# Kernel optimization log

Hardware: AMD Instinct MI355X
Metric: run time of the kernel (lower is better)

The kernel has to match this reference:

```python
import jax, jax.numpy as jnp
import numpy as np

M_MAX = 8
GN_GROUPS = 8  # _pick_gn_groups(64)
HEADS = 4
G_C = 19
PER_C = 16


def silu(x):
    return x * jax.nn.sigmoid(x)


def layer_norm(x, g, b, eps=1e-5):
    mu = x.mean(-1, keepdims=True)
    var = ((x - mu) ** 2).mean(-1, keepdims=True)
    return (x - mu) * jax.lax.rsqrt(var + eps) * g + b


def group_norm(x, g, b, eps=1e-5):
    N, C, H, W = x.shape
    xr = x.reshape(N, GN_GROUPS, C // GN_GROUPS, H, W)
    mu = xr.mean((2, 3, 4), keepdims=True)
    var = ((xr - mu) ** 2).mean((2, 3, 4), keepdims=True)
    xn = ((xr - mu) * jax.lax.rsqrt(var + eps)).reshape(N, C, H, W)
    return xn * g[:, None, None] + b[:, None, None]


def conv1x1(x, w):  # x [N,C,H,W], w [O,C]
    return jnp.einsum('nchw,oc->nohw', x, w)


def dw3x3(x, w):  # depthwise 3x3, w [C,1,3,3]
    return jax.lax.conv_general_dilated(x, w, (1, 1), 'SAME', feature_group_count=x.shape[1], dimension_numbers=('NCHW', 'OIHW', 'NCHW'))


def forward(board, stem_w, stem_g, stem_b, qw, qb, kw, kb, vw, vb, ow, ob, ln_g, ln_b, dw_w, gn1_g, gn1_b, pw_w, gn2_g, gn2_b, pol_w, pol_b, vh_w1, vh_b1, vh_w2, vh_b2, om_w, om_b, op_w1, op_b1, op_w2, op_b2):
    B, Cin, H, W = board.shape
    hid = stem_w.shape[0]
    hd = hid // HEADS
    g = board[:, :G_C]
    p = board[:, G_C:G_C + M_MAX * PER_C].reshape(B, M_MAX, PER_C, H, W)
    player_in = jnp.concatenate([jnp.broadcast_to(g[:, None], (B, M_MAX, G_C, H, W)), p], axis=2)
    x = conv1x1(player_in.reshape(B * M_MAX, G_C + PER_C, H, W), stem_w)
    x = silu(group_norm(x, stem_g, stem_b)).reshape(B, M_MAX, hid, H, W)
    m_each = jnp.argmax(board[:, 7:14, 0, 0], axis=1) + 2  # number of players in [2,8]
    present = jnp.arange(M_MAX) < m_each[:, None]  # [B, M_MAX] bool
    neg = jnp.finfo(board.dtype).min
    L = qw.shape[0]
    for i in range(L):
        tokens = x.transpose(0, 3, 4, 1, 2).reshape(B, H * W, M_MAX, hid)
        q = (tokens @ qw[i].T + qb[i]).reshape(B, H * W, M_MAX, HEADS, hd)
        k = (tokens @ kw[i].T + kb[i]).reshape(B, H * W, M_MAX, HEADS, hd)
        v = (tokens @ vw[i].T + vb[i]).reshape(B, H * W, M_MAX, HEADS, hd)
        logits = jnp.einsum('bnqhd,bnkhd->bnhqk', q, k) * (hd ** -0.5)
        logits = jnp.where(present[:, None, None, None, :], logits, neg)
        attn = jax.nn.softmax(logits, axis=-1)
        ao = jnp.einsum('bnhqk,bnkhd->bnqhd', attn, v).reshape(B, H * W, M_MAX, hid)
        tokens = layer_norm(tokens + ao @ ow[i].T + ob[i], ln_g[i], ln_b[i])
        xc = tokens.reshape(B, H, W, M_MAX, hid).transpose(0, 3, 4, 1, 2).reshape(B * M_MAX, hid, H, W)
        y = silu(group_norm(dw3x3(xc, dw_w[i]), gn1_g[i], gn1_b[i]))
        y = group_norm(conv1x1(y, pw_w[i]), gn2_g[i], gn2_b[i])
        xc = silu(xc + y)
        x = xc.reshape(B, M_MAX, hid, H, W) * present[:, :, None, None, None].astype(xc.dtype)
    x0 = x[:, 0]
    logits_p = (conv1x1(x0, pol_w) + pol_b[:, None, None]).reshape(B, H * W)
    pooled0 = x0.mean((2, 3))
    value = (silu(pooled0 @ vh_w1.T + vh_b1) @ vh_w2.T + vh_b2)[:, 0]
    move_all = (conv1x1(x.reshape(B * M_MAX, hid, H, W), om_w) + om_b[:, None, None]).reshape(B, M_MAX, M_MAX, H * W)
    pooled_all = x.mean((3, 4))
    param_all = (silu(pooled_all @ op_w1.T + op_b1) @ op_w2.T + op_b2).reshape(B, M_MAX, M_MAX, 5)
    idx = jnp.arange(M_MAX)
    pf = present[..., None]
    opp_move = move_all[:, idx, idx, :] * pf.astype(move_all.dtype)
    opp_param = param_all[:, idx, idx, :] * pf.astype(param_all.dtype)
    return (logits_p, value, opp_move, opp_param)


def setup_inputs() -> dict:
    key = jax.random.key(0)
    ks = iter(jax.random.split(key, 48))
    def rn(shape, s=0.1):
        return jax.random.normal(next(ks), shape, jnp.float32) * s
    B, H, W, C, L = 16, 32, 32, 64, 6
    inp = {
        'board': jax.random.normal(next(ks), (B, 149, H, W), jnp.float32),
        'stem_w': rn((C, 35)), 'stem_g': jnp.ones((C,)), 'stem_b': jnp.zeros((C,)),
        'qw': rn((L, C, C)), 'qb': rn((L, C), 0.01),
        'kw': rn((L, C, C)), 'kb': rn((L, C), 0.01),
        'vw': rn((L, C, C)), 'vb': rn((L, C), 0.01),
        'ow': rn((L, C, C)), 'ob': rn((L, C), 0.01),
        'ln_g': jnp.ones((L, C)), 'ln_b': jnp.zeros((L, C)),
        'dw_w': rn((L, C, 1, 3, 3)),
        'gn1_g': jnp.ones((L, C)), 'gn1_b': jnp.zeros((L, C)),
        'pw_w': rn((L, C, C)),
        'gn2_g': jnp.ones((L, C)), 'gn2_b': jnp.zeros((L, C)),
        'pol_w': rn((1, C)), 'pol_b': jnp.zeros((1,)),
        'vh_w1': rn((C, C)), 'vh_b1': jnp.zeros((C,)),
        'vh_w2': rn((1, C)), 'vh_b2': jnp.zeros((1,)),
        'om_w': rn((M_MAX, C)), 'om_b': jnp.zeros((M_MAX,)),
        'op_w1': rn((C, C)), 'op_b1': jnp.zeros((C,)),
        'op_w2': rn((M_MAX * 5, C)), 'op_b2': jnp.zeros((M_MAX * 5,)),
    }
    return inp


def reference(board, stem_w, stem_g, stem_b, qw, qb, kw, kb, vw, vb, ow, ob, ln_g, ln_b, dw_w, gn1_g, gn1_b, pw_w, gn2_g, gn2_b, pol_w, pol_b, vh_w1, vh_b1, vh_w2, vh_b2, om_w, om_b, op_w1, op_b1, op_w2, op_b2):
    return forward(board, stem_w, stem_g, stem_b, qw, qb, kw, kb, vw, vb, ow, ob, ln_g, ln_b, dw_w, gn1_g, gn1_b, pw_w, gn2_g, gn2_b, pol_w, pol_b, vh_w1, vh_b1, vh_w2, vh_b2, om_w, om_b, op_w1, op_b1, op_w2, op_b2)
```

## Files before the change

kernel.cpp:

```cpp
#include <hip/hip_runtime.h>
#include <cstddef>


#define WSX   0u
#define WST   8388608u
#define WSY   16777216u
#define WSS   25165824u
#define WSP   (WSS + 26624u)
#define WSPL  (WSP + 128u)

#define ATTN_LDS_BYTES ((4 * 64 * 64 + 8 * 64 * 8) * 4)

__device__ __forceinline__ float silu_f(float x) { return x / (1.f + __expf(-x)); }

__device__ __forceinline__ float wsum64(float v) {
#pragma unroll
  for (int s = 1; s < 64; s <<= 1) v += __shfl_xor(v, s);
  return v;
}

__device__ __forceinline__ float bcastlane(float v, int l) {
  return __int_as_float(__builtin_amdgcn_readlane(__float_as_int(v), l));
}

__device__ __forceinline__ float rowsum16(float v) {
  v += __int_as_float(__builtin_amdgcn_update_dpp(0, __float_as_int(v), 0x128, 0xf, 0xf, true));
  v += __int_as_float(__builtin_amdgcn_update_dpp(0, __float_as_int(v), 0x124, 0xf, 0xf, true));
  v += __int_as_float(__builtin_amdgcn_update_dpp(0, __float_as_int(v), 0x122, 0xf, 0xf, true));
  v += __int_as_float(__builtin_amdgcn_update_dpp(0, __float_as_int(v), 0x121, 0xf, 0xf, true));
  return v;
}

__device__ __forceinline__ float wsum64b(float v) {
  v = rowsum16(v);
  v += __shfl_xor(v, 16);
  v += __shfl_xor(v, 32);
  return v;
}

__global__ __launch_bounds__(256) void k_init(const float* __restrict__ board,
                                              float* __restrict__ ws) {
  int tid = threadIdx.x;
  for (unsigned i = blockIdx.x * 256 + tid; i < 26624u; i += 64u * 256u) ws[WSS + i] = 0.f;
  if (blockIdx.x == 0 && tid < 128) {
    int b = tid >> 3, m = tid & 7;
    float best = board[(size_t)(b * 149 + 7) * 1024];
    int bi = 0;
    for (int ch = 1; ch < 7; ++ch) {
      float v = board[(size_t)(b * 149 + 7 + ch) * 1024];
      if (v > best) { best = v; bi = ch; }
    }
    int m_each = bi + 2;
    ws[WSP + tid] = (m < m_each) ? 1.f : 0.f;
  }
}

__global__ __launch_bounds__(256) void k_stem(const float* __restrict__ board,
                                              const float* __restrict__ stem_w,
                                              float* __restrict__ ws) {
  __shared__ float A[147 * 64];
  __shared__ float WT[35 * 64];
  __shared__ float red_s[256], red_ss[256];
  int tid = threadIdx.x;
  int b = blockIdx.x >> 4, n0 = (blockIdx.x & 15) * 64;
  for (int i = tid; i < 147 * 64; i += 256) {
    int c = i >> 6, p = i & 63;
    A[i] = board[(size_t)(b * 149 + c) * 1024 + n0 + p];
  }
  for (int i = tid; i < 35 * 64; i += 256) {
    int o = i / 35, c = i % 35;
    WT[c * 64 + o] = stem_w[i];
  }
  __syncthreads();
  int o = tid & 63, wv = tid >> 6;
  float* X = ws + WSX;
  float st_s[8], st_ss[8];
#pragma unroll
  for (int m = 0; m < 8; ++m) { st_s[m] = 0.f; st_ss[m] = 0.f; }
  for (int m = 0; m < 8; ++m) {
    for (int k = 0; k < 4; ++k) {
      int q = wv + 4 * k;
      float a0 = 0.f, a1 = 0.f, a2 = 0.f, a3 = 0.f;
#pragma unroll
      for (int c = 0; c < 19; ++c) {
        float w = WT[c * 64 + o];
        float4 av = *(const float4*)&A[c * 64 + q * 4];
        a0 += av.x * w; a1 += av.y * w; a2 += av.z * w; a3 += av.w * w;
      }
#pragma unroll
      for (int j = 0; j < 16; ++j) {
        float w = WT[(19 + j) * 64 + o];
        float4 av = *(const float4*)&A[(19 + m * 16 + j) * 64 + q * 4];
        a0 += av.x * w; a1 += av.y * w; a2 += av.z * w; a3 += av.w * w;
      }
      int n = n0 + q * 4;
      float vals[4] = {a0, a1, a2, a3};
#pragma unroll
      for (int j = 0; j < 4; ++j) {
        X[((size_t)(b * 1024 + n + j) * 8 + m) * 64 + o] = vals[j];
        st_s[m] += vals[j];
        st_ss[m] += vals[j] * vals[j];
      }
    }
  }
  float* stats = ws + WSS;
  for (int m = 0; m < 8; ++m) {
    __syncthreads();
    red_s[tid] = st_s[m];
    red_ss[tid] = st_ss[m];
    __syncthreads();
    if (tid < 8) {
      float a = 0.f, a2 = 0.f;
      for (int w4 = 0; w4 < 4; ++w4)
        for (int j = 0; j < 8; ++j) {
          int t2 = w4 * 64 + tid * 8 + j;
          a += red_s[t2]; a2 += red_ss[t2];
        }
      atomicAdd(&stats[((b * 8 + m) * 8 + tid) * 2 + 0], a);
      atomicAdd(&stats[((b * 8 + m) * 8 + tid) * 2 + 1], a2);
    }
  }
}

__global__ __launch_bounds__(256) void k_gn_silu(float* __restrict__ X,
                                                 const float* __restrict__ g,
                                                 const float* __restrict__ bt,
                                                 const float* __restrict__ stats) {
  for (size_t idx = (size_t)blockIdx.x * 256 + threadIdx.x; idx < 8388608ull;
       idx += (size_t)2048 * 256) {
    int c = (int)(idx & 63);
    int m = (int)((idx >> 6) & 7);
    int b = (int)(idx >> 19);
    int gi = ((b * 8 + m) * 8 + (c >> 3)) * 2;
    float s = stats[gi], s2 = stats[gi + 1];
    float mean = s * (1.f / 8192.f);
    float var = s2 * (1.f / 8192.f) - mean * mean;
    float rstd = rsqrtf(var + 1e-5f);
    float v = (X[idx] - mean) * rstd * g[c] + bt[c];
    X[idx] = silu_f(v);
  }
}

#define FMA8(acc, WW)                                                      \
  acc[0] += t0.x * (WW); acc[1] += t0.y * (WW); acc[2] += t0.z * (WW);     \
  acc[3] += t0.w * (WW); acc[4] += t1.x * (WW); acc[5] += t1.y * (WW);     \
  acc[6] += t1.z * (WW); acc[7] += t1.w * (WW);

__global__ __launch_bounds__(512, 4) void k_attn(
    const float* __restrict__ Xin, const float* __restrict__ Yin,
    const float* __restrict__ s2p, const float* __restrict__ g2p,
    const float* __restrict__ b2p, float* __restrict__ T,
    const float* __restrict__ qw, const float* __restrict__ qb,
    const float* __restrict__ kw, const float* __restrict__ kb,
    const float* __restrict__ vw, const float* __restrict__ vb,
    const float* __restrict__ ow, const float* __restrict__ ob,
    const float* __restrict__ lng, const float* __restrict__ lnb,
    const float* __restrict__ present, int fused) {
  extern __shared__ float sm[];
  float* Wq = sm;
  float* Wk = sm + 4096;
  float* Wv = sm + 8192;
  float* Wo = sm + 12288;
  float* BUF = sm + 16384;
  int tid = threadIdx.x;
  int lane = tid & 63, wv = tid >> 6;
  int b = blockIdx.x >> 5;
  int n0 = (blockIdx.x & 31) * 32;
  for (int i = tid; i < 4096; i += 512) {
    int o = i >> 6, c = i & 63;
    Wq[c * 64 + o] = qw[i];
    Wk[c * 64 + o] = kw[i];
    Wv[c * 64 + o] = vw[i];
    Wo[c * 64 + o] = ow[i];
  }
  float bq = qb[lane], bk = kb[lane], bv = vb[lane], bo = ob[lane];
  float gl = lng[lane], bl = lnb[lane];
  unsigned pmask = 0;
#pragma unroll
  for (int m = 0; m < 8; ++m) pmask |= (present[b * 8 + m] > 0.5f) ? (1u << m) : 0u;
  float Ag[8], Bg[8];
  if (fused) {
    int g = lane >> 3;
    float gw = g2p[lane], bw_ = b2p[lane];
#pragma unroll
    for (int m = 0; m < 8; ++m) {
      int gi = ((b * 8 + m) * 8 + g) * 2;
      float sg = s2p[gi], sg2 = s2p[gi + 1];
      float mean = sg * (1.f / 8192.f);
      float var = sg2 * (1.f / 8192.f) - mean * mean;
      float rstd = rsqrtf(var + 1e-5f);
      Ag[m] = rstd * gw;
      Bg[m] = bw_ - mean * Ag[m];
    }
  }
  __syncthreads();
  float* bw = BUF + wv * 512;
  const int sw = lane & 12;
  for (int j = 0; j < 4; ++j) {
    int n = n0 + wv * 4 + j;
    size_t pbase = ((size_t)(b * 1024 + n) * 8) * 64 + lane;
    float tok[8];
    if (fused) {
#pragma unroll
      for (int m = 0; m < 8; ++m) {
        float tv = Xin[pbase + m * 64];
        float yv = Yin[pbase + m * 64];
        float z = tv + (yv * Ag[m] + Bg[m]);
        float pres = ((pmask >> m) & 1) ? 1.f : 0.f;
        tok[m] = silu_f(z) * pres;
      }
    } else {
#pragma unroll
      for (int m = 0; m < 8; ++m) tok[m] = Xin[pbase + m * 64];
    }
    float aq[8], ak[8], av[8];
#pragma unroll
    for (int m = 0; m < 8; ++m) { aq[m] = bq; ak[m] = bk; av[m] = bv; }
#pragma unroll 16
    for (int c = 0; c < 64; ++c) {
      float wq_ = Wq[c * 64 + lane];
      float wk_ = Wk[c * 64 + lane];
      float wv_ = Wv[c * 64 + lane];
#pragma unroll
      for (int m = 0; m < 8; ++m) {
        float t = bcastlane(tok[m], c);
        aq[m] = fmaf(t, wq_, aq[m]);
        ak[m] = fmaf(t, wk_, ak[m]);
        av[m] = fmaf(t, wv_, av[m]);
      }
    }
    float ao[8];
#pragma unroll
    for (int mq = 0; mq < 8; ++mq) {
      float lg[8];
#pragma unroll
      for (int mk = 0; mk < 8; ++mk)
        lg[mk] = rowsum16(aq[mq] * ak[mk]) * 0.25f;
      float mx = -3.0e38f;
#pragma unroll
      for (int mk = 0; mk < 8; ++mk)
        if ((pmask >> mk) & 1) mx = fmaxf(mx, lg[mk]);
      float se = 0.f, acc = 0.f;
#pragma unroll
      for (int mk = 0; mk < 8; ++mk) {
        float e = ((pmask >> mk) & 1) ? __expf(lg[mk] - mx) : 0.f;
        se += e;
        acc += e * av[mk];
      }
      ao[mq] = acc * __builtin_amdgcn_rcpf(se);
    }
    *(float4*)&bw[(lane * 8) ^ sw]     = make_float4(ao[0], ao[1], ao[2], ao[3]);
    *(float4*)&bw[(lane * 8 + 4) ^ sw] = make_float4(ao[4], ao[5], ao[6], ao[7]);
    __asm__ volatile("" ::: "memory");
    float z[8];
#pragma unroll
    for (int m = 0; m < 8; ++m) z[m] = bo;
#pragma unroll 16
    for (int c = 0; c < 64; ++c) {
      float4 t0 = *(const float4*)&bw[(c * 8) ^ (c & 12)];
      float4 t1 = *(const float4*)&bw[(c * 8 + 4) ^ (c & 12)];
      float wo_ = Wo[c * 64 + lane];
      FMA8(z, wo_)
    }
    __asm__ volatile("" ::: "memory");
    float* tp = T + pbase;
#pragma unroll
    for (int m = 0; m < 8; ++m) {
      float r = tok[m] + z[m];
      float mean = wsum64b(r) * (1.f / 64.f);
      float d = r - mean;
      float var = wsum64b(d * d) * (1.f / 64.f);
      float rstd = rsqrtf(var + 1e-5f);
      tp[m * 64] = d * rstd * gl + bl;
    }
  }
}

__global__ __launch_bounds__(256) void k_dw(const float* __restrict__ T, float* __restrict__ Y,
                                            const float* __restrict__ dww,
                                            float* __restrict__ stats) {
  __shared__ float red_s[256], red_ss[256];
  int tid = threadIdx.x, lane = tid & 63, wv = tid >> 6;
  int bm = blockIdx.x >> 3, rg = blockIdx.x & 7;
  int b = bm >> 3, m = bm & 7;
  int r = rg * 4 + wv;
  float w9[9];
#pragma unroll
  for (int k = 0; k < 9; ++k) w9[k] = dww[lane * 9 + k];
  float s = 0.f, ss = 0.f;
  const size_t base = (size_t)b * 1024 * 512 + (size_t)m * 64 + lane;
  for (int col = 0; col < 32; ++col) {
    float acc = 0.f;
#pragma unroll
    for (int dh = -1; dh <= 1; ++dh) {
      int rr = r + dh;
      if (rr < 0 || rr > 31) continue;
#pragma unroll
      for (int dx = -1; dx <= 1; ++dx) {
        int cc = col + dx;
        if (cc < 0 || cc > 31) continue;
        acc += T[base + (size_t)(rr * 32 + cc) * 512] * w9[(dh + 1) * 3 + dx + 1];
      }
    }
    Y[base + (size_t)(r * 32 + col) * 512] = acc;
    s += acc;
    ss += acc * acc;
  }
  red_s[tid] = s;
  red_ss[tid] = ss;
  __syncthreads();
  if (tid < 8) {
    float a = 0.f, a2 = 0.f;
    for (int w4 = 0; w4 < 4; ++w4)
      for (int j = 0; j < 8; ++j) {
        int t2 = w4 * 64 + tid * 8 + j;
        a += red_s[t2]; a2 += red_ss[t2];
      }
    atomicAdd(&stats[(bm * 8 + tid) * 2 + 0], a);
    atomicAdd(&stats[(bm * 8 + tid) * 2 + 1], a2);
  }
}

__global__ __launch_bounds__(256) void k_pw(float* __restrict__ Y, const float* __restrict__ pw,
                                            const float* __restrict__ g1,
                                            const float* __restrict__ b1,
                                            const float* __restrict__ s1,
                                            float* __restrict__ s2) {
  __shared__ float PWT[4096];
  __shared__ float HB[4][256];
  __shared__ float red_s[256], red_ss[256];
  int tid = threadIdx.x, lane = tid & 63, wv = tid >> 6;
  int bm = blockIdx.x >> 2, pt = blockIdx.x & 3;
  int b = bm >> 3, m = bm & 7;
  int n0 = pt * 256;
  for (int i = tid; i < 4096; i += 256) {
    int o = i >> 6, c = i & 63;
    PWT[c * 64 + o] = pw[i];
  }
  int g = lane >> 3;
  float sg = s1[(bm * 8 + g) * 2], sg2 = s1[(bm * 8 + g) * 2 + 1];
  float mean = sg * (1.f / 8192.f);
  float var = sg2 * (1.f / 8192.f) - mean * mean;
  float rstd = rsqrtf(var + 1e-5f);
  float A = rstd * g1[lane];
  float Bc = b1[lane] - mean * A;
  __syncthreads();
  float st = 0.f, st2 = 0.f;
  const size_t base = (size_t)b * 1024 * 512 + (size_t)m * 64 + lane;
  for (int it = 0; it < 16; ++it) {
    int n = n0 + it * 16 + wv * 4;
    float h[4];
#pragma unroll
    for (int jj = 0; jj < 4; ++jj) {
      float y = Y[base + (size_t)(n + jj) * 512];
      h[jj] = silu_f(y * A + Bc);
    }
    *(float4*)&HB[wv][lane * 4] = make_float4(h[0], h[1], h[2], h[3]);
    __asm__ volatile("" ::: "memory");
    float a0 = 0.f, a1 = 0.f, a2 = 0.f, a3 = 0.f;
#pragma unroll 8
    for (int c = 0; c < 64; ++c) {
      float4 hh = *(const float4*)&HB[wv][c * 4];
      float w = PWT[c * 64 + lane];
      a0 += hh.x * w; a1 += hh.y * w; a2 += hh.z * w; a3 += hh.w * w;
    }
    float vals[4] = {a0, a1, a2, a3};
#pragma unroll
    for (int jj = 0; jj < 4; ++jj) {
      Y[base + (size_t)(n + jj) * 512] = vals[jj];
      st += vals[jj];
      st2 += vals[jj] * vals[jj];
    }
    __asm__ volatile("" ::: "memory");
  }
  red_s[tid] = st;
  red_ss[tid] = st2;
  __syncthreads();
  if (tid < 8) {
    float a = 0.f, a2 = 0.f;
    for (int w4 = 0; w4 < 4; ++w4)
      for (int j = 0; j < 8; ++j) {
        int t2 = w4 * 64 + tid * 8 + j;
        a += red_s[t2]; a2 += red_ss[t2];
      }
    atomicAdd(&s2[(bm * 8 + tid) * 2 + 0], a);
    atomicAdd(&s2[(bm * 8 + tid) * 2 + 1], a2);
  }
}

__global__ __launch_bounds__(256) void k_fuse(const float* __restrict__ T,
                                              const float* __restrict__ Y,
                                              float* __restrict__ X,
                                              const float* __restrict__ g2,
                                              const float* __restrict__ b2,
                                              const float* __restrict__ s2,
                                              const float* __restrict__ present) {
  int tid = threadIdx.x, lane = tid & 63, wv = tid >> 6;
  int bm = blockIdx.x >> 3, pt = blockIdx.x & 7;
  int b = bm >> 3, m = bm & 7;
  int g = lane >> 3;
  float sg = s2[(bm * 8 + g) * 2], sg2 = s2[(bm * 8 + g) * 2 + 1];
  float mean = sg * (1.f / 8192.f);
  float var = sg2 * (1.f / 8192.f) - mean * mean;
  float rstd = rsqrtf(var + 1e-5f);
  float A = rstd * g2[lane];
  float Bc = b2[lane] - mean * A;
  float pres = present[bm];
  const size_t base = (size_t)b * 1024 * 512 + (size_t)m * 64 + lane;
  int n0 = pt * 128;
  for (int i2 = 0; i2 < 32; ++i2) {
    int n = n0 + i2 * 4 + wv;
    size_t idx = base + (size_t)n * 512;
    float z = T[idx] + (Y[idx] * A + Bc);
    X[idx] = silu_f(z) * pres;
  }
}

__global__ __launch_bounds__(256) void k_heads_px(const float* __restrict__ X,
                                                  const float* __restrict__ pol_w,
                                                  const float* __restrict__ pol_b,
                                                  const float* __restrict__ om_w,
                                                  const float* __restrict__ om_b,
                                                  const float* __restrict__ present,
                                                  float* __restrict__ out) {
  int tid = threadIdx.x, lane = tid & 63, wv = tid >> 6;
  int b = blockIdx.x >> 4, n0 = (blockIdx.x & 15) * 64;
  float pw_ = pol_w[lane];
  for (int it = 0; it < 16; ++it) {
    int n = n0 + wv * 16 + it;
    const float* xp = X + ((size_t)(b * 1024 + n) * 8) * 64 + lane;
#pragma unroll
    for (int m = 0; m < 8; ++m) {
      float v = xp[m * 64];
      float d = wsum64(v * om_w[m * 64 + lane]);
      if (m == 0) {
        float dp = wsum64(v * pw_);
        if (lane == 0) out[b * 1024 + n] = dp + pol_b[0];
      }
      if (lane == 0)
        out[16400u + (size_t)(b * 8 + m) * 1024 + n] = (d + om_b[m]) * present[b * 8 + m];
    }
  }
}

__global__ __launch_bounds__(256) void k_pool(const float* __restrict__ X,
                                              float* __restrict__ pooled) {
  __shared__ float red[256];
  int tid = threadIdx.x, lane = tid & 63, wv = tid >> 6;
  int b = blockIdx.x >> 3, m = blockIdx.x & 7;
  float s = 0.f;
  for (int p = wv; p < 1024; p += 4)
    s += X[((size_t)(b * 1024 + p) * 8 + m) * 64 + lane];
  red[tid] = s;
  __syncthreads();
  if (tid < 64)
    pooled[(b * 8 + m) * 64 + tid] =
        (red[tid] + red[tid + 64] + red[tid + 128] + red[tid + 192]) * (1.f / 1024.f);
}

__global__ __launch_bounds__(64) void k_heads_vec(
    const float* __restrict__ pooled, const float* __restrict__ vh_w1,
    const float* __restrict__ vh_b1, const float* __restrict__ vh_w2,
    const float* __restrict__ vh_b2, const float* __restrict__ op_w1,
    const float* __restrict__ op_b1, const float* __restrict__ op_w2,
    const float* __restrict__ op_b2, const float* __restrict__ present,
    float* __restrict__ out) {
  int lane = threadIdx.x;
  int b = blockIdx.x >> 3, m = blockIdx.x & 7;
  const float* pp = pooled + (b * 8 + m) * 64;
  float h = op_b1[lane];
  for (int c = 0; c < 64; ++c) h += pp[c] * op_w1[lane * 64 + c];
  h = silu_f(h);
  float pres = present[b * 8 + m];
  for (int jj = 0; jj < 5; ++jj) {
    float d = wsum64(h * op_w2[(m * 5 + jj) * 64 + lane]);
    if (lane == 0) out[147472u + (b * 8 + m) * 5 + jj] = (d + op_b2[m * 5 + jj]) * pres;
  }
  if (m == 0) {
    float hv = vh_b1[lane];
    for (int c = 0; c < 64; ++c) hv += pp[c] * vh_w1[lane * 64 + c];
    hv = silu_f(hv);
    float dv = wsum64(hv * vh_w2[lane]);
    if (lane == 0) out[16384u + b] = dv + vh_b2[0];
  }
}

extern "C" void kernel_launch(void* const* d_in, const int* in_sizes, int n_in,
                              void* d_out, int out_size, void* d_ws, size_t ws_size,
                              hipStream_t stream) {
  const float* board  = (const float*)d_in[0];
  const float* stem_w = (const float*)d_in[1];
  const float* stem_g = (const float*)d_in[2];
  const float* stem_b = (const float*)d_in[3];
  const float* qw = (const float*)d_in[4];
  const float* qb = (const float*)d_in[5];
  const float* kw = (const float*)d_in[6];
  const float* kb = (const float*)d_in[7];
  const float* vw = (const float*)d_in[8];
  const float* vb = (const float*)d_in[9];
  const float* ow = (const float*)d_in[10];
  const float* ob = (const float*)d_in[11];
  const float* ln_g = (const float*)d_in[12];
  const float* ln_b = (const float*)d_in[13];
  const float* dw_w = (const float*)d_in[14];
  const float* gn1_g = (const float*)d_in[15];
  const float* gn1_b = (const float*)d_in[16];
  const float* pw_w = (const float*)d_in[17];
  const float* gn2_g = (const float*)d_in[18];
  const float* gn2_b = (const float*)d_in[19];
  const float* pol_w = (const float*)d_in[20];
  const float* pol_b = (const float*)d_in[21];
  const float* vh_w1 = (const float*)d_in[22];
  const float* vh_b1 = (const float*)d_in[23];
  const float* vh_w2 = (const float*)d_in[24];
  const float* vh_b2 = (const float*)d_in[25];
  const float* om_w = (const float*)d_in[26];
  const float* om_b = (const float*)d_in[27];
  const float* op_w1 = (const float*)d_in[28];
  const float* op_b1 = (const float*)d_in[29];
  const float* op_w2 = (const float*)d_in[30];
  const float* op_b2 = (const float*)d_in[31];
  float* ws = (float*)d_ws;
  float* out = (float*)d_out;

  (void)hipFuncSetAttribute((const void*)k_attn,
                            hipFuncAttributeMaxDynamicSharedMemorySize,
                            ATTN_LDS_BYTES);

  k_init<<<64, 256, 0, stream>>>(board, ws);
  k_stem<<<256, 256, 0, stream>>>(board, stem_w, ws);
  k_gn_silu<<<2048, 256, 0, stream>>>(ws + WSX, stem_g, stem_b, ws + WSS);

  for (int i = 0; i < 6; ++i) {
    float* s1 = ws + WSS + (size_t)(1 + 2 * i) * 2048;
    float* s2 = ws + WSS + (size_t)(2 + 2 * i) * 2048;
    if (i == 0) {
      k_attn<<<512, 512, ATTN_LDS_BYTES, stream>>>(
          ws + WSX, ws + WSX, ws + WSS, gn2_g, gn2_b, ws + WST,
          qw, qb, kw, kb, vw, vb, ow, ob, ln_g, ln_b, ws + WSP, 0);
    } else {
      float* s2prev = ws + WSS + (size_t)(2 * i) * 2048;
      k_attn<<<512, 512, ATTN_LDS_BYTES, stream>>>(
          ws + WST, ws + WSY, s2prev, gn2_g + (i - 1) * 64, gn2_b + (i - 1) * 64,
          ws + WST, qw + i * 4096, qb + i * 64, kw + i * 4096, kb + i * 64,
          vw + i * 4096, vb + i * 64, ow + i * 4096, ob + i * 64, ln_g + i * 64,
          ln_b + i * 64, ws + WSP, 1);
    }
    k_dw<<<1024, 256, 0, stream>>>(ws + WST, ws + WSY, dw_w + i * 576, s1);
    k_pw<<<512, 256, 0, stream>>>(ws + WSY, pw_w + i * 4096, gn1_g + i * 64,
                                  gn1_b + i * 64, s1, s2);
  }
  k_fuse<<<1024, 256, 0, stream>>>(ws + WST, ws + WSY, ws + WSX, gn2_g + 5 * 64,
                                   gn2_b + 5 * 64, ws + WSS + (size_t)12 * 2048,
                                   ws + WSP);

  k_heads_px<<<256, 256, 0, stream>>>(ws + WSX, pol_w, pol_b, om_w, om_b, ws + WSP, out);
  k_pool<<<128, 256, 0, stream>>>(ws + WSX, ws + WSPL);
  k_heads_vec<<<128, 64, 0, stream>>>(ws + WSPL, vh_w1, vh_b1, vh_w2, vh_b2, op_w1,
                                      op_b1, op_w2, op_b2, ws + WSP, out);
}
```

Before: 1.548 ms.

## Stage attention tokens in LDS and vectorize depthwise conv over channel quads

In the attention kernel the per-token channel broadcasts, previously done with readlane, now come from an LDS buffer that is read as float4 vectors, and the QKV and output projection loops are fully unrolled. The depthwise conv kernel is rebuilt so each thread handles four channels of one player with float4 loads and stores, and each block covers one board row across all players. The launch count is halved and the group-stat reduction is remapped to match. The intent is fewer scalar and readlane instructions and wider memory accesses, at the cost of more LDS traffic and a possible rise in register pressure from full unrolling.

```diff
diff --git a/kernel.cpp b/kernel.cpp
--- a/kernel.cpp
+++ b/kernel.cpp
@@ -17,10 +17,6 @@
 #pragma unroll
   for (int s = 1; s < 64; s <<= 1) v += __shfl_xor(v, s);
   return v;
-}
-
-__device__ __forceinline__ float bcastlane(float v, int l) {
-  return __int_as_float(__builtin_amdgcn_readlane(__float_as_int(v), l));
 }
 
 __device__ __forceinline__ float rowsum16(float v) {
@@ -213,21 +209,22 @@
 #pragma unroll
       for (int m = 0; m < 8; ++m) tok[m] = Xin[pbase + m * 64];
     }
+    *(float4*)&bw[(lane * 8) ^ sw]     = make_float4(tok[0], tok[1], tok[2], tok[3]);
+    *(float4*)&bw[(lane * 8 + 4) ^ sw] = make_float4(tok[4], tok[5], tok[6], tok[7]);
+    __asm__ volatile("" ::: "memory");
     float aq[8], ak[8], av[8];
 #pragma unroll
     for (int m = 0; m < 8; ++m) { aq[m] = bq; ak[m] = bk; av[m] = bv; }
-#pragma unroll 16
+#pragma unroll
     for (int c = 0; c < 64; ++c) {
+      float4 t0 = *(const float4*)&bw[(c * 8) ^ (c & 12)];
+      float4 t1 = *(const float4*)&bw[(c * 8 + 4) ^ (c & 12)];
       float wq_ = Wq[c * 64 + lane];
       float wk_ = Wk[c * 64 + lane];
       float wv_ = Wv[c * 64 + lane];
-#pragma unroll
-      for (int m = 0; m < 8; ++m) {
-        float t = bcastlane(tok[m], c);
-        aq[m] = fmaf(t, wq_, aq[m]);
-        ak[m] = fmaf(t, wk_, ak[m]);
-        av[m] = fmaf(t, wv_, av[m]);
-      }
+      FMA8(aq, wq_)
+      FMA8(ak, wk_)
+      FMA8(av, wv_)
     }
     float ao[8];
 #pragma unroll
@@ -249,13 +246,14 @@
       }
       ao[mq] = acc * __builtin_amdgcn_rcpf(se);
     }
+    __asm__ volatile("" ::: "memory");
     *(float4*)&bw[(lane * 8) ^ sw]     = make_float4(ao[0], ao[1], ao[2], ao[3]);
     *(float4*)&bw[(lane * 8 + 4) ^ sw] = make_float4(ao[4], ao[5], ao[6], ao[7]);
     __asm__ volatile("" ::: "memory");
     float z[8];
 #pragma unroll
     for (int m = 0; m < 8; ++m) z[m] = bo;
-#pragma unroll 16
+#pragma unroll
     for (int c = 0; c < 64; ++c) {
       float4 t0 = *(const float4*)&bw[(c * 8) ^ (c & 12)];
       float4 t1 = *(const float4*)&bw[(c * 8 + 4) ^ (c & 12)];
@@ -280,17 +278,24 @@
                                             const float* __restrict__ dww,
                                             float* __restrict__ stats) {
   __shared__ float red_s[256], red_ss[256];
-  int tid = threadIdx.x, lane = tid & 63, wv = tid >> 6;
-  int bm = blockIdx.x >> 3, rg = blockIdx.x & 7;
-  int b = bm >> 3, m = bm & 7;
-  int r = rg * 4 + wv;
-  float w9[9];
-#pragma unroll
-  for (int k = 0; k < 9; ++k) w9[k] = dww[lane * 9 + k];
+  int tid = threadIdx.x;
+  int b = blockIdx.x >> 5, r = blockIdx.x & 31;
+  int half = tid >> 7;
+  int mc4 = tid & 127;
+  int m = mc4 >> 4, c4 = mc4 & 15, c0 = c4 * 4;
+  float4 w9[9];
+#pragma unroll
+  for (int t = 0; t < 9; ++t) {
+    w9[t].x = dww[(c0 + 0) * 9 + t];
+    w9[t].y = dww[(c0 + 1) * 9 + t];
+    w9[t].z = dww[(c0 + 2) * 9 + t];
+    w9[t].w = dww[(c0 + 3) * 9 + t];
+  }
   float s = 0.f, ss = 0.f;
-  const size_t base = (size_t)b * 1024 * 512 + (size_t)m * 64 + lane;
-  for (int col = 0; col < 32; ++col) {
-    float acc = 0.f;
+  const size_t plane = (size_t)b * 524288 + (size_t)m * 64 + c0;
+  for (int ci = 0; ci < 16; ++ci) {
+    int col = half * 16 + ci;
+    float4 acc = make_float4(0.f, 0.f, 0.f, 0.f);
 #pragma unroll
     for (int dh = -1; dh <= 1; ++dh) {
       int rr = r + dh;
@@ -299,25 +304,32 @@
       for (int dx = -1; dx <= 1; ++dx) {
         int cc = col + dx;
         if (cc < 0 || cc > 31) continue;
-        acc += T[base + (size_t)(rr * 32 + cc) * 512] * w9[(dh + 1) * 3 + dx + 1];
-      }
-    }
-    Y[base + (size_t)(r * 32 + col) * 512] = acc;
-    s += acc;
-    ss += acc * acc;
+        float4 tv = *(const float4*)&T[plane + (size_t)(rr * 32 + cc) * 512];
+        float4 w = w9[(dh + 1) * 3 + dx + 1];
+        acc.x += tv.x * w.x; acc.y += tv.y * w.y;
+        acc.z += tv.z * w.z; acc.w += tv.w * w.w;
+      }
+    }
+    *(float4*)&Y[plane + (size_t)(r * 32 + col) * 512] = acc;
+    s += acc.x + acc.y + acc.z + acc.w;
+    ss += acc.x * acc.x + acc.y * acc.y + acc.z * acc.z + acc.w * acc.w;
   }
   red_s[tid] = s;
   red_ss[tid] = ss;
   __syncthreads();
-  if (tid < 8) {
+  if (tid < 64) {
+    int mm = tid >> 3, g = tid & 7;
     float a = 0.f, a2 = 0.f;
-    for (int w4 = 0; w4 < 4; ++w4)
-      for (int j = 0; j < 8; ++j) {
-        int t2 = w4 * 64 + tid * 8 + j;
-        a += red_s[t2]; a2 += red_ss[t2];
-      }
-    atomicAdd(&stats[(bm * 8 + tid) * 2 + 0], a);
-    atomicAdd(&stats[(bm * 8 + tid) * 2 + 1], a2);
+#pragma unroll
+    for (int hh = 0; hh < 2; ++hh)
+#pragma unroll
+      for (int e = 0; e < 2; ++e) {
+        int idx = hh * 128 + mm * 16 + g * 2 + e;
+        a += red_s[idx];
+        a2 += red_ss[idx];
+      }
+    atomicAdd(&stats[((b * 8 + mm) * 8 + g) * 2 + 0], a);
+    atomicAdd(&stats[((b * 8 + mm) * 8 + g) * 2 + 1], a2);
   }
 }
 
@@ -546,7 +558,7 @@
           vw + i * 4096, vb + i * 64, ow + i * 4096, ob + i * 64, ln_g + i * 64,
           ln_b + i * 64, ws + WSP, 1);
     }
-    k_dw<<<1024, 256, 0, stream>>>(ws + WST, ws + WSY, dw_w + i * 576, s1);
+    k_dw<<<512, 256, 0, stream>>>(ws + WST, ws + WSY, dw_w + i * 576, s1);
     k_pw<<<512, 256, 0, stream>>>(ws + WSY, pw_w + i * 4096, gn1_g + i * 64,
                                   gn1_b + i * 64, s1, s2);
   }
```

Result: faster. 1.411 ms (-8.8%).
